# Kernel tuning notes

Measured on AMD Instinct MI355X. Metric: run time of the kernel, lower is better.

The kernel has to match this reference:

```python
import jax, jax.numpy as jnp
import numpy as np

B, IN, H1, H2, OUT, P = 8192, 1024, 2048, 2048, 1024, 8


def setup_inputs() -> dict:
    key = jax.random.key(0)
    ks = jax.random.split(key, 12)
    s = 0.02
    return {
        "x": jax.random.normal(ks[0], (B, IN), dtype=jnp.float32),
        # layer 1: P expert linears (stacked) + selector
        "W1": jax.random.normal(ks[1], (P, IN, H1), dtype=jnp.float32) * s,
        "b1": jax.random.normal(ks[2], (P, H1), dtype=jnp.float32) * s,
        "S1": jax.random.normal(ks[3], (IN, P), dtype=jnp.float32) * s,
        "sb1": jax.random.normal(ks[4], (P,), dtype=jnp.float32) * s,
        # layer 2
        "W2": jax.random.normal(ks[5], (P, H1, H2), dtype=jnp.float32) * s,
        "b2": jax.random.normal(ks[6], (P, H2), dtype=jnp.float32) * s,
        "S2": jax.random.normal(ks[7], (H1, P), dtype=jnp.float32) * s,
        "sb2": jax.random.normal(ks[8], (P,), dtype=jnp.float32) * s,
        # classifier
        "Wc": jax.random.normal(ks[9], (H2, OUT), dtype=jnp.float32) * s,
        "bc": jax.random.normal(ks[10], (OUT,), dtype=jnp.float32) * s,
    }


def _drn_layer(x, W, b, S, sb):
    # selector + softmax routing probs: [B, P]
    probs = jax.nn.softmax(x @ S + sb, axis=-1)
    # all-expert dense outputs: [B, P, O]
    outs = jnp.einsum('bi,pio->bpo', x, W) + b[None, :, :]
    # soft-weighted combine over experts
    return jnp.einsum('bpo,bp->bo', outs, probs)


def reference(x, W1, b1, S1, sb1, W2, b2, S2, sb2, Wc, bc):
    h = jax.nn.relu(_drn_layer(x, W1, b1, S1, sb1))
    h = jax.nn.relu(_drn_layer(h, W2, b2, S2, sb2))
    return h @ Wc + bc
```

## Files before the change

kernel.cpp:

```cpp
#include <hip/hip_runtime.h>
#include <hip/hip_bf16.h>

#define B_SZ   8192
#define IN_SZ  1024
#define H1_SZ  2048
#define H2_SZ  2048
#define OUT_SZ 1024
#define NP     8

typedef __bf16 bf16x8 __attribute__((ext_vector_type(8)));
typedef float  f32x4  __attribute__((ext_vector_type(4)));

__device__ __forceinline__ void async_ld16(const void* g, void* l) {
    __builtin_amdgcn_global_load_lds(
        (const __attribute__((address_space(1))) unsigned int*)g,
        (__attribute__((address_space(3))) unsigned int*)l,
        16, 0, 0);
}

__global__ void cast_bf16_k(const float* __restrict__ in, __hip_bfloat16* __restrict__ out) {
    size_t i = ((size_t)blockIdx.x * 256 + threadIdx.x) * 8;
    float4 f0 = *(const float4*)(in + i);
    float4 f1 = *(const float4*)(in + i + 4);
    __hip_bfloat16 t[8] = {
        __float2bfloat16(f0.x), __float2bfloat16(f0.y),
        __float2bfloat16(f0.z), __float2bfloat16(f0.w),
        __float2bfloat16(f1.x), __float2bfloat16(f1.y),
        __float2bfloat16(f1.z), __float2bfloat16(f1.w)};
    uint4 u4;
    __builtin_memcpy(&u4, t, 16);
    *(uint4*)(out + i) = u4;
}

__global__ void transpose_cast_k(const float* __restrict__ in, __hip_bfloat16* __restrict__ out,
                                 int K, int N) {
    __shared__ float tile[32][33];
    int n0 = blockIdx.x * 32, k0 = blockIdx.y * 32;
    int tx = threadIdx.x, ty = threadIdx.y;
#pragma unroll
    for (int j = 0; j < 4; ++j)
        tile[ty + j * 8][tx] = in[(size_t)(k0 + ty + j * 8) * N + (n0 + tx)];
    __syncthreads();
    const int kk = (tx & 15) * 2;
#pragma unroll
    for (int j = 0; j < 2; ++j) {
        int nn = ty + j * 8 + (tx >> 4) * 16;
        __hip_bfloat16 t2[2] = {__float2bfloat16(tile[kk][nn]),
                                __float2bfloat16(tile[kk + 1][nn])};
        unsigned int u;
        __builtin_memcpy(&u, t2, 4);
        *(unsigned int*)(out + (size_t)(n0 + nn) * K + (k0 + kk)) = u;
    }
}

template <typename T>
__global__ void selector_k(const T* __restrict__ in, const float* __restrict__ S,
                           const float* __restrict__ sb, float* __restrict__ probs,
                           float* __restrict__ ratT, int K) {
    int row  = blockIdx.x * blockDim.y + threadIdx.y;
    int lane = threadIdx.x;
    float acc[NP];
#pragma unroll
    for (int p = 0; p < NP; ++p) acc[p] = 0.f;
    const T* xr = in + (size_t)row * K;
    for (int k = lane; k < K; k += 64) {
        float xv;
        if constexpr (sizeof(T) == 2) xv = __bfloat162float(xr[k]);
        else                          xv = (float)xr[k];
        const float* sr = S + (size_t)k * NP;
#pragma unroll
        for (int p = 0; p < NP; ++p) acc[p] += xv * sr[p];
    }
#pragma unroll
    for (int p = 0; p < NP; ++p)
#pragma unroll
        for (int off = 32; off > 0; off >>= 1)
            acc[p] += __shfl_down(acc[p], off, 64);
    if (lane == 0) {
        float v[NP], m = -1e30f;
#pragma unroll
        for (int p = 0; p < NP; ++p) { v[p] = acc[p] + sb[p]; m = fmaxf(m, v[p]); }
        float s = 0.f;
#pragma unroll
        for (int p = 0; p < NP; ++p) { v[p] = expf(v[p] - m); s += v[p]; }
        float inv = 1.f / s;
#pragma unroll
        for (int p = 0; p < NP; ++p) probs[(size_t)row * NP + p] = v[p] * inv;
#pragma unroll
        for (int p = 0; p < NP - 1; ++p) ratT[(size_t)p * B_SZ + row] = v[p] / v[p + 1];
        ratT[(size_t)(NP - 1) * B_SZ + row] = v[NP - 1] * inv;
    }
}

template <int TPS>
__global__ __launch_bounds__(512, 2)
void drn_gemm8_k(const __hip_bfloat16* __restrict__ A, const __hip_bfloat16* __restrict__ Wt,
                 int N, int K, int Kin, const float* __restrict__ ratT,
                 const float* __restrict__ probs, const float* __restrict__ bexp,
                 __hip_bfloat16* __restrict__ C) {
    __shared__ alignas(16) char smem[131072];

    const int tid  = threadIdx.x;
    const int wid  = tid >> 6, lane = tid & 63;
    const int quad = lane >> 4, l16 = lane & 15;
    const int wr = wid >> 2, wc = wid & 3;

    const int g   = blockIdx.x;
    const int cpx = gridDim.x >> 3;
    const int wg  = (g & 7) * cpx + (g >> 3);
    const int nbn = N >> 8;
    const int mb  = wg / nbn, nb = wg % nbn;
    const int m0  = mb * 256, n0 = nb * 256;

    const int arow = tid >> 3;
    const int gsw  = ((tid & 7) ^ (arow & 7)) << 3;
    const __hip_bfloat16* Ag = A  + (size_t)(m0 + arow) * Kin + gsw;
    const __hip_bfloat16* Bg = Wt + (size_t)(n0 + arow) * K + gsw;
    const size_t r64a = (size_t)64 * Kin;
    const size_t r64b = (size_t)64 * K;
    char* aDst = smem + wid * 1024;
    char* bDst = smem + 65536 + wid * 1024;

#define STG_A(dbuf, ksrc, h) do {                                              \
    const __hip_bfloat16* s_ = Ag + (((ksrc) & (TPS - 1)) * 64) + (size_t)(2*(h)) * r64a; \
    char* d_ = aDst + (dbuf) * 32768 + (h) * 16384;                            \
    async_ld16(s_,        d_);                                                 \
    async_ld16(s_ + r64a, d_ + 8192); } while (0)
#define STG_B(dbuf, ksrc, h) do {                                              \
    const __hip_bfloat16* s_ = Bg + ((size_t)(ksrc) * 64) + (size_t)(2*(h)) * r64b; \
    char* d_ = bDst + (dbuf) * 32768 + (h) * 16384;                            \
    async_ld16(s_,        d_);                                                 \
    async_ld16(s_ + r64b, d_ + 8192); } while (0)

    const int csw  = (quad ^ (l16 & 7)) << 4;
    const int aoff = (wr * 128 + l16) * 128 + csw;
    const int boff = 65536 + (wc * 64 + l16) * 128 + csw;

#define LDA(dst, dbuf, m, k) dst = *(const bf16x8*)(smem + (dbuf) * 32768 + ((aoff ^ ((k) << 6)) + (m) * 2048))
#define LDB(dst, dbuf, n, k) dst = *(const bf16x8*)(smem + (dbuf) * 32768 + ((boff ^ ((k) << 6)) + (n) * 2048))

#define LD_A2(dbuf, mq)                               \
    LDA(af[0][0], dbuf, 2*(mq),     0); LDA(af[0][1], dbuf, 2*(mq),     1); \
    LDA(af[1][0], dbuf, 2*(mq) + 1, 0); LDA(af[1][1], dbuf, 2*(mq) + 1, 1)
#define LD_B8(dbuf)                                   \
    LDB(bfr[0][0], dbuf, 0, 0); LDB(bfr[0][1], dbuf, 0, 1); \
    LDB(bfr[1][0], dbuf, 1, 0); LDB(bfr[1][1], dbuf, 1, 1); \
    LDB(bfr[2][0], dbuf, 2, 0); LDB(bfr[2][1], dbuf, 2, 1); \
    LDB(bfr[3][0], dbuf, 3, 0); LDB(bfr[3][1], dbuf, 3, 1)

#define PH_SYNC()                                          \
    __builtin_amdgcn_s_barrier();                          \
    asm volatile("s_waitcnt lgkmcnt(0)" ::: "memory");     \
    __builtin_amdgcn_sched_barrier(0)

#define PH_MFMA(q) do {                                    \
    __builtin_amdgcn_s_setprio(1);                         \
    _Pragma("unroll")                                      \
    for (int ml = 0; ml < 2; ++ml)                         \
      _Pragma("unroll")                                    \
      for (int n_ = 0; n_ < 4; ++n_)                       \
        _Pragma("unroll")                                  \
        for (int k_ = 0; k_ < 2; ++k_)                     \
          acc[2*(q)+ml][n_] = __builtin_amdgcn_mfma_f32_16x16x32_bf16( \
              af[ml][k_], bfr[n_][k_], acc[2*(q)+ml][n_], 0, 0, 0);    \
    __builtin_amdgcn_s_setprio(0); } while (0)

#define PH_END()                                           \
    __builtin_amdgcn_s_barrier();                          \
    __builtin_amdgcn_sched_barrier(0)

#define PH_END_VM()                                        \
    asm volatile("s_waitcnt vmcnt(4)" ::: "memory");       \
    __builtin_amdgcn_s_barrier();                          \
    __builtin_amdgcn_sched_barrier(0)

    f32x4 zero = {0.f, 0.f, 0.f, 0.f};
    f32x4 acc[8][4];
#pragma unroll
    for (int m = 0; m < 8; ++m)
#pragma unroll
        for (int n = 0; n < 4; ++n) acc[m][n] = zero;

    const int NT = K >> 6;
    const int NI = NT >> 1;

    STG_A(0, 0, 0); STG_A(0, 0, 1);
    STG_B(0, 0, 0); STG_B(0, 0, 1);
    STG_B(1, 1, 0); STG_B(1, 1, 1);
    asm volatile("s_waitcnt vmcnt(4)" ::: "memory");
    __builtin_amdgcn_s_barrier();
    __builtin_amdgcn_sched_barrier(0);

    bf16x8 af[2][2], bfr[4][2];

    for (int i = 0; i < NI; ++i) {
        const int T  = 2 * i;
        const int k2 = (T + 2 < NT) ? T + 2 : NT - 1;
        const int k3 = (T + 3 < NT) ? T + 3 : NT - 1;

        LD_B8(0); LD_A2(0, 0);
        STG_A(1, T + 1, 0);
        PH_SYNC(); PH_MFMA(0); PH_END();

        LD_A2(0, 1);
        STG_A(1, T + 1, 1);
        PH_SYNC(); PH_MFMA(1); PH_END();

        LD_A2(0, 2);
        STG_B(0, k2, 0);
        PH_SYNC(); PH_MFMA(2); PH_END();

        LD_A2(0, 3);
        STG_B(0, k2, 1);
        PH_SYNC(); PH_MFMA(3); PH_END_VM();

        LD_B8(1); LD_A2(1, 0);
        STG_A(0, k2, 0);
        PH_SYNC(); PH_MFMA(0); PH_END();

        LD_A2(1, 1);
        STG_A(0, k2, 1);
        PH_SYNC(); PH_MFMA(1); PH_END();

        LD_A2(1, 2);
        STG_B(1, k3, 0);
        PH_SYNC(); PH_MFMA(2); PH_END();

        LD_A2(1, 3);
        STG_B(1, k3, 1);
        PH_SYNC(); PH_MFMA(3); PH_END_VM();

        if (((i + 1) & (TPS / 2 - 1)) == 0) {
            const int p = (i + 1) / (TPS / 2) - 1;
            const float* rp = ratT + (size_t)p * B_SZ + (m0 + wr * 128 + quad * 4);
            f32x4 rr[8];
#pragma unroll
            for (int m = 0; m < 8; ++m) rr[m] = *(const f32x4*)(rp + m * 16);
#pragma unroll
            for (int m = 0; m < 8; ++m)
#pragma unroll
                for (int n = 0; n < 4; ++n)
                    acc[m][n] *= rr[m];
        }
    }

    asm volatile("s_waitcnt vmcnt(0)" ::: "memory");

    const int colb = n0 + wc * 64 + l16;
    float bx[4][NP];
#pragma unroll
    for (int n = 0; n < 4; ++n)
#pragma unroll
        for (int p = 0; p < NP; ++p)
            bx[n][p] = bexp[(size_t)p * N + colb + n * 16];
#pragma unroll
    for (int m = 0; m < 8; ++m) {
#pragma unroll
        for (int r = 0; r < 4; ++r) {
            const int row = m0 + wr * 128 + m * 16 + quad * 4 + r;
            const float* pr = probs + (size_t)row * NP;
            f32x4 p0 = *(const f32x4*)pr;
            f32x4 p1 = *(const f32x4*)(pr + 4);
            float pv[NP] = {p0[0], p0[1], p0[2], p0[3], p1[0], p1[1], p1[2], p1[3]};
#pragma unroll
            for (int n = 0; n < 4; ++n) {
                float bsum = 0.f;
#pragma unroll
                for (int p = 0; p < NP; ++p) bsum += pv[p] * bx[n][p];
                float v = fmaxf(acc[m][n][r] + bsum, 0.f);
                C[(size_t)row * N + colb + n * 16] = __float2bfloat16(v);
            }
        }
    }
#undef STG_A
#undef STG_B
#undef LDA
#undef LDB
#undef LD_A2
#undef LD_B8
#undef PH_SYNC
#undef PH_MFMA
#undef PH_END
#undef PH_END_VM
}

__global__ __launch_bounds__(256)
void gemm_bt_k(const __hip_bfloat16* __restrict__ A, const __hip_bfloat16* __restrict__ Bt,
               int M, int N, int K, const float* __restrict__ bias, float* __restrict__ C) {
    __shared__ alignas(16) __hip_bfloat16 As[2 * 128 * 32];
    __shared__ alignas(16) __hip_bfloat16 Bs[2 * 128 * 32];
    const int tid  = threadIdx.x;
    const int wid  = tid >> 6, lane = tid & 63;
    const int quad = lane >> 4, l16 = lane & 15;
    const int waveM = (wid >> 1) << 6, waveN = (wid & 1) << 6;
    const int m0 = blockIdx.x * 128, n0 = blockIdx.y * 128;

    f32x4 zero = {0.f, 0.f, 0.f, 0.f};
    f32x4 acc[4][4];
#pragma unroll
    for (int a = 0; a < 4; ++a)
#pragma unroll
        for (int b = 0; b < 4; ++b) acc[a][b] = zero;

    const int srow = tid >> 2;
    const int skc  = (((tid & 3) ^ (srow & 3) ^ ((srow >> 2) & 3)) << 3);
    const __hip_bfloat16* Ag = A  + (size_t)(m0 + srow) * K + skc;
    const __hip_bfloat16* Bg = Bt + (size_t)(n0 + srow) * K + skc;
    const size_t rowStep = (size_t)64 * K;
    __hip_bfloat16* AsB = As + wid * 512;
    __hip_bfloat16* BsB = Bs + wid * 512;
    const int csel = (quad ^ (l16 & 3) ^ ((l16 >> 2) & 3)) << 3;

    async_ld16(Ag,           AsB);
    async_ld16(Ag + rowStep, AsB + 2048);
    async_ld16(Bg,           BsB);
    async_ld16(Bg + rowStep, BsB + 2048);

    for (int kt = 0; kt < K; kt += 32) {
        const int cur = (kt >> 5) & 1;
        __syncthreads();
        if (kt + 32 < K) {
            const int nb = (1 - cur) * 4096;
            async_ld16(Ag + kt + 32,           AsB + nb);
            async_ld16(Ag + kt + 32 + rowStep, AsB + nb + 2048);
            async_ld16(Bg + kt + 32,           BsB + nb);
            async_ld16(Bg + kt + 32 + rowStep, BsB + nb + 2048);
        }
        const __hip_bfloat16* AsC = As + cur * 4096;
        const __hip_bfloat16* BsC = Bs + cur * 4096;
        bf16x8 af[4], bfr[4];
#pragma unroll
        for (int q = 0; q < 4; ++q) {
            af[q]  = *(const bf16x8*)(AsC + (waveM + q * 16 + l16) * 32 + csel);
            bfr[q] = *(const bf16x8*)(BsC + (waveN + q * 16 + l16) * 32 + csel);
        }
#pragma unroll
        for (int tm = 0; tm < 4; ++tm)
#pragma unroll
            for (int tn = 0; tn < 4; ++tn)
                acc[tm][tn] = __builtin_amdgcn_mfma_f32_16x16x32_bf16(
                    af[tm], bfr[tn], acc[tm][tn], 0, 0, 0);
    }

    const int colb = n0 + waveN + l16;
#pragma unroll
    for (int tm = 0; tm < 4; ++tm)
#pragma unroll
        for (int r = 0; r < 4; ++r) {
            int row = m0 + waveM + tm * 16 + quad * 4 + r;
#pragma unroll
            for (int tn = 0; tn < 4; ++tn)
                C[(size_t)row * N + colb + tn * 16] =
                    acc[tm][tn][r] + bias[colb + tn * 16];
        }
}

extern "C" void kernel_launch(void* const* d_in, const int* in_sizes, int n_in,
                              void* d_out, int out_size, void* d_ws, size_t ws_size,
                              hipStream_t stream) {
    const float* x   = (const float*)d_in[0];
    const float* W1  = (const float*)d_in[1];
    const float* b1  = (const float*)d_in[2];
    const float* S1  = (const float*)d_in[3];
    const float* sb1 = (const float*)d_in[4];
    const float* W2  = (const float*)d_in[5];
    const float* b2  = (const float*)d_in[6];
    const float* S2  = (const float*)d_in[7];
    const float* sb2 = (const float*)d_in[8];
    const float* Wc  = (const float*)d_in[9];
    const float* bc  = (const float*)d_in[10];
    float* out = (float*)d_out;

    char* ws = (char*)d_ws;
    size_t off = 0;
    auto alloc = [&](size_t bytes) {
        char* p = ws + off;
        off += (bytes + 255) & ~(size_t)255;
        return p;
    };
    __hip_bfloat16* W1t = (__hip_bfloat16*)alloc((size_t)H1_SZ * (NP * IN_SZ) * 2);
    __hip_bfloat16* W2t = (__hip_bfloat16*)alloc((size_t)H2_SZ * (NP * H1_SZ) * 2);
    __hip_bfloat16* Wct = (__hip_bfloat16*)alloc((size_t)OUT_SZ * H2_SZ * 2);
    float* probs1       = (float*)alloc((size_t)B_SZ * NP * 4);
    float* probs2       = (float*)alloc((size_t)B_SZ * NP * 4);
    float* rat1         = (float*)alloc((size_t)NP * B_SZ * 4);
    float* rat2         = (float*)alloc((size_t)NP * B_SZ * 4);
    __hip_bfloat16* xbf = (__hip_bfloat16*)alloc((size_t)B_SZ * IN_SZ * 2);
    __hip_bfloat16* h1  = (__hip_bfloat16*)alloc((size_t)B_SZ * H1_SZ * 2);
    __hip_bfloat16* h2  = (__hip_bfloat16*)alloc((size_t)B_SZ * H2_SZ * 2);

    dim3 tb(32, 8);
    transpose_cast_k<<<dim3(H1_SZ / 32, (NP * IN_SZ) / 32), tb, 0, stream>>>(W1, W1t, NP * IN_SZ, H1_SZ);
    transpose_cast_k<<<dim3(H2_SZ / 32, (NP * H1_SZ) / 32), tb, 0, stream>>>(W2, W2t, NP * H1_SZ, H2_SZ);
    transpose_cast_k<<<dim3(OUT_SZ / 32, H2_SZ / 32), tb, 0, stream>>>(Wc, Wct, H2_SZ, OUT_SZ);
    cast_bf16_k<<<(B_SZ * IN_SZ) / (256 * 8), 256, 0, stream>>>(x, xbf);

    selector_k<float><<<B_SZ / 4, dim3(64, 4), 0, stream>>>(x, S1, sb1, probs1, rat1, IN_SZ);
    drn_gemm8_k<16><<<(B_SZ / 256) * (H1_SZ / 256), 512, 0, stream>>>(
        xbf, W1t, H1_SZ, NP * IN_SZ, IN_SZ, rat1, probs1, b1, h1);

    selector_k<__hip_bfloat16><<<B_SZ / 4, dim3(64, 4), 0, stream>>>(h1, S2, sb2, probs2, rat2, H1_SZ);
    drn_gemm8_k<32><<<(B_SZ / 256) * (H2_SZ / 256), 512, 0, stream>>>(
        h1, W2t, H2_SZ, NP * H1_SZ, H1_SZ, rat2, probs2, b2, h2);

    gemm_bt_k<<<dim3(B_SZ / 128, OUT_SZ / 128), 256, 0, stream>>>(
        h2, Wct, B_SZ, OUT_SZ, H2_SZ, bc, out);
}
```

Before: 1.036 ms.

## Double-buffer LDS fragment loads in DRN GEMM and merge prep kernels

Restructures the main DRN GEMM loop to ping-pong A and B register fragments, so the LDS reads for the next MFMA phase are issued before the current phase's MFMAs. It replaces the per-phase lgkmcnt(0) wait with finer-grained vmcnt waits. It also folds the three weight transpose-casts and the input cast into one prep kernel launch to cut launch overhead. In exchange the kernel uses more VGPRs for the doubled fragments, and the looser waits make the ordering of async LDS fills against reads harder to get right.

```diff
diff --git a/kernel.cpp b/kernel.cpp
--- a/kernel.cpp
+++ b/kernel.cpp
@@ -18,24 +18,11 @@
         16, 0, 0);
 }
 
-__global__ void cast_bf16_k(const float* __restrict__ in, __hip_bfloat16* __restrict__ out) {
-    size_t i = ((size_t)blockIdx.x * 256 + threadIdx.x) * 8;
-    float4 f0 = *(const float4*)(in + i);
-    float4 f1 = *(const float4*)(in + i + 4);
-    __hip_bfloat16 t[8] = {
-        __float2bfloat16(f0.x), __float2bfloat16(f0.y),
-        __float2bfloat16(f0.z), __float2bfloat16(f0.w),
-        __float2bfloat16(f1.x), __float2bfloat16(f1.y),
-        __float2bfloat16(f1.z), __float2bfloat16(f1.w)};
-    uint4 u4;
-    __builtin_memcpy(&u4, t, 16);
-    *(uint4*)(out + i) = u4;
-}
-
-__global__ void transpose_cast_k(const float* __restrict__ in, __hip_bfloat16* __restrict__ out,
-                                 int K, int N) {
-    __shared__ float tile[32][33];
-    int n0 = blockIdx.x * 32, k0 = blockIdx.y * 32;
+__device__ __forceinline__ void transpose_body(float (*tile)[33],
+                                               const float* __restrict__ in,
+                                               __hip_bfloat16* __restrict__ out,
+                                               int K, int N, int bx, int by) {
+    int n0 = bx * 32, k0 = by * 32;
     int tx = threadIdx.x, ty = threadIdx.y;
 #pragma unroll
     for (int j = 0; j < 4; ++j)
@@ -50,6 +37,46 @@
         unsigned int u;
         __builtin_memcpy(&u, t2, 4);
         *(unsigned int*)(out + (size_t)(n0 + nn) * K + (k0 + kk)) = u;
+    }
+}
+
+__global__ void prep_k(const float* __restrict__ W1, const float* __restrict__ W2,
+                       const float* __restrict__ Wc, const float* __restrict__ x,
+                       __hip_bfloat16* __restrict__ W1t, __hip_bfloat16* __restrict__ W2t,
+                       __hip_bfloat16* __restrict__ Wct, __hip_bfloat16* __restrict__ xbf) {
+    __shared__ float tile[32][33];
+    int id = blockIdx.x;
+    const int nA = (H1_SZ / 32) * ((NP * IN_SZ) / 32);
+    const int nB = (H2_SZ / 32) * ((NP * H1_SZ) / 32);
+    const int nC = (OUT_SZ / 32) * (H2_SZ / 32);
+    if (id < nA) {
+        transpose_body(tile, W1, W1t, NP * IN_SZ, H1_SZ, id % (H1_SZ / 32), id / (H1_SZ / 32));
+        return;
+    }
+    id -= nA;
+    if (id < nB) {
+        transpose_body(tile, W2, W2t, NP * H1_SZ, H2_SZ, id % (H2_SZ / 32), id / (H2_SZ / 32));
+        return;
+    }
+    id -= nB;
+    if (id < nC) {
+        transpose_body(tile, Wc, Wct, H2_SZ, OUT_SZ, id % (OUT_SZ / 32), id / (OUT_SZ / 32));
+        return;
+    }
+    id -= nC;
+    {
+        int t = threadIdx.y * 32 + threadIdx.x;
+        size_t i = ((size_t)id * 256 + t) * 8;
+        float4 f0 = *(const float4*)(x + i);
+        float4 f1 = *(const float4*)(x + i + 4);
+        __hip_bfloat16 tt[8] = {
+            __float2bfloat16(f0.x), __float2bfloat16(f0.y),
+            __float2bfloat16(f0.z), __float2bfloat16(f0.w),
+            __float2bfloat16(f1.x), __float2bfloat16(f1.y),
+            __float2bfloat16(f1.z), __float2bfloat16(f1.w)};
+        uint4 u4;
+        __builtin_memcpy(&u4, tt, 16);
+        *(uint4*)(xbf + i) = u4;
     }
 }
 
@@ -139,21 +166,20 @@
 #define LDA(dst, dbuf, m, k) dst = *(const bf16x8*)(smem + (dbuf) * 32768 + ((aoff ^ ((k) << 6)) + (m) * 2048))
 #define LDB(dst, dbuf, n, k) dst = *(const bf16x8*)(smem + (dbuf) * 32768 + ((boff ^ ((k) << 6)) + (n) * 2048))
 
-#define LD_A2(dbuf, mq)                               \
-    LDA(af[0][0], dbuf, 2*(mq),     0); LDA(af[0][1], dbuf, 2*(mq),     1); \
-    LDA(af[1][0], dbuf, 2*(mq) + 1, 0); LDA(af[1][1], dbuf, 2*(mq) + 1, 1)
-#define LD_B8(dbuf)                                   \
-    LDB(bfr[0][0], dbuf, 0, 0); LDB(bfr[0][1], dbuf, 0, 1); \
-    LDB(bfr[1][0], dbuf, 1, 0); LDB(bfr[1][1], dbuf, 1, 1); \
-    LDB(bfr[2][0], dbuf, 2, 0); LDB(bfr[2][1], dbuf, 2, 1); \
-    LDB(bfr[3][0], dbuf, 3, 0); LDB(bfr[3][1], dbuf, 3, 1)
-
-#define PH_SYNC()                                          \
+#define LD_AF(dst, dbuf, mq)                               \
+    LDA(dst[0][0], dbuf, 2*(mq),     0); LDA(dst[0][1], dbuf, 2*(mq),     1); \
+    LDA(dst[1][0], dbuf, 2*(mq) + 1, 0); LDA(dst[1][1], dbuf, 2*(mq) + 1, 1)
+#define LD_BF(dst, dbuf, kk)                               \
+    LDB(dst[0][kk], dbuf, 0, kk); LDB(dst[1][kk], dbuf, 1, kk); \
+    LDB(dst[2][kk], dbuf, 2, kk); LDB(dst[3][kk], dbuf, 3, kk)
+
+#define BAR()                                              \
     __builtin_amdgcn_s_barrier();                          \
-    asm volatile("s_waitcnt lgkmcnt(0)" ::: "memory");     \
     __builtin_amdgcn_sched_barrier(0)
 
-#define PH_MFMA(q) do {                                    \
+#define VMW(n) asm volatile("s_waitcnt vmcnt(" #n ")" ::: "memory")
+
+#define MF16(afX, bfrX, q) do {                            \
     __builtin_amdgcn_s_setprio(1);                         \
     _Pragma("unroll")                                      \
     for (int ml = 0; ml < 2; ++ml)                         \
@@ -162,17 +188,8 @@
         _Pragma("unroll")                                  \
         for (int k_ = 0; k_ < 2; ++k_)                     \
           acc[2*(q)+ml][n_] = __builtin_amdgcn_mfma_f32_16x16x32_bf16( \
-              af[ml][k_], bfr[n_][k_], acc[2*(q)+ml][n_], 0, 0, 0);    \
+              afX[ml][k_], bfrX[n_][k_], acc[2*(q)+ml][n_], 0, 0, 0);  \
     __builtin_amdgcn_s_setprio(0); } while (0)
-
-#define PH_END()                                           \
-    __builtin_amdgcn_s_barrier();                          \
-    __builtin_amdgcn_sched_barrier(0)
-
-#define PH_END_VM()                                        \
-    asm volatile("s_waitcnt vmcnt(4)" ::: "memory");       \
-    __builtin_amdgcn_s_barrier();                          \
-    __builtin_amdgcn_sched_barrier(0)
 
     f32x4 zero = {0.f, 0.f, 0.f, 0.f};
     f32x4 acc[8][4];
@@ -187,48 +204,49 @@
     STG_A(0, 0, 0); STG_A(0, 0, 1);
     STG_B(0, 0, 0); STG_B(0, 0, 1);
     STG_B(1, 1, 0); STG_B(1, 1, 1);
-    asm volatile("s_waitcnt vmcnt(4)" ::: "memory");
-    __builtin_amdgcn_s_barrier();
-    __builtin_amdgcn_sched_barrier(0);
-
-    bf16x8 af[2][2], bfr[4][2];
+    VMW(4);
+    BAR();
+    bf16x8 afA[2][2], afB[2][2], bfrA[4][2], bfrB[4][2];
+    LD_BF(bfrA, 0, 0); LD_BF(bfrA, 0, 1);
+    LD_AF(afA, 0, 0);
 
     for (int i = 0; i < NI; ++i) {
         const int T  = 2 * i;
         const int k2 = (T + 2 < NT) ? T + 2 : NT - 1;
         const int k3 = (T + 3 < NT) ? T + 3 : NT - 1;
 
-        LD_B8(0); LD_A2(0, 0);
         STG_A(1, T + 1, 0);
-        PH_SYNC(); PH_MFMA(0); PH_END();
-
-        LD_A2(0, 1);
+        LD_AF(afB, 0, 1);
+        BAR(); MF16(afA, bfrA, 0); BAR();
         STG_A(1, T + 1, 1);
-        PH_SYNC(); PH_MFMA(1); PH_END();
-
-        LD_A2(0, 2);
+        VMW(4);
+        LD_AF(afA, 0, 2);
+        BAR(); MF16(afB, bfrA, 1); BAR();
         STG_B(0, k2, 0);
-        PH_SYNC(); PH_MFMA(2); PH_END();
-
-        LD_A2(0, 3);
+        VMW(2);
+        LD_AF(afB, 0, 3);
+        LD_BF(bfrB, 1, 0);
+        BAR(); MF16(afA, bfrA, 2); BAR();
         STG_B(0, k2, 1);
-        PH_SYNC(); PH_MFMA(3); PH_END_VM();
-
-        LD_B8(1); LD_A2(1, 0);
+        LD_AF(afA, 1, 0);
+        LD_BF(bfrB, 1, 1);
+        BAR(); MF16(afB, bfrA, 3); BAR();
         STG_A(0, k2, 0);
-        PH_SYNC(); PH_MFMA(0); PH_END();
-
-        LD_A2(1, 1);
+        LD_AF(afB, 1, 1);
+        BAR(); MF16(afA, bfrB, 0); BAR();
         STG_A(0, k2, 1);
-        PH_SYNC(); PH_MFMA(1); PH_END();
-
-        LD_A2(1, 2);
+        VMW(4);
+        LD_AF(afA, 1, 2);
+        BAR(); MF16(afB, bfrB, 1); BAR();
         STG_B(1, k3, 0);
-        PH_SYNC(); PH_MFMA(2); PH_END();
-
-        LD_A2(1, 3);
+        VMW(2);
+        LD_AF(afB, 1, 3);
+        LD_BF(bfrA, 0, 0);
+        BAR(); MF16(afA, bfrB, 2); BAR();
         STG_B(1, k3, 1);
-        PH_SYNC(); PH_MFMA(3); PH_END_VM();
+        LD_AF(afA, 0, 0);
+        LD_BF(bfrA, 0, 1);
+        BAR(); MF16(afB, bfrB, 3); BAR();
 
         if (((i + 1) & (TPS / 2 - 1)) == 0) {
             const int p = (i + 1) / (TPS / 2) - 1;
@@ -276,12 +294,11 @@
 #undef STG_B
 #undef LDA
 #undef LDB
-#undef LD_A2
-#undef LD_B8
-#undef PH_SYNC
-#undef PH_MFMA
-#undef PH_END
-#undef PH_END_VM
+#undef LD_AF
+#undef LD_BF
+#undef BAR
+#undef VMW
+#undef MF16
 }
 
 __global__ __launch_bounds__(256)
@@ -389,11 +406,11 @@
     __hip_bfloat16* h1  = (__hip_bfloat16*)alloc((size_t)B_SZ * H1_SZ * 2);
     __hip_bfloat16* h2  = (__hip_bfloat16*)alloc((size_t)B_SZ * H2_SZ * 2);
 
-    dim3 tb(32, 8);
-    transpose_cast_k<<<dim3(H1_SZ / 32, (NP * IN_SZ) / 32), tb, 0, stream>>>(W1, W1t, NP * IN_SZ, H1_SZ);
-    transpose_cast_k<<<dim3(H2_SZ / 32, (NP * H1_SZ) / 32), tb, 0, stream>>>(W2, W2t, NP * H1_SZ, H2_SZ);
-    transpose_cast_k<<<dim3(OUT_SZ / 32, H2_SZ / 32), tb, 0, stream>>>(Wc, Wct, H2_SZ, OUT_SZ);
-    cast_bf16_k<<<(B_SZ * IN_SZ) / (256 * 8), 256, 0, stream>>>(x, xbf);
+    const int nPrep = (H1_SZ / 32) * ((NP * IN_SZ) / 32)
+                    + (H2_SZ / 32) * ((NP * H1_SZ) / 32)
+                    + (OUT_SZ / 32) * (H2_SZ / 32)
+                    + (B_SZ * IN_SZ) / (256 * 8);
+    prep_k<<<nPrep, dim3(32, 8), 0, stream>>>(W1, W2, Wc, x, W1t, W2t, Wct, xbf);
 
     selector_k<float><<<B_SZ / 4, dim3(64, 4), 0, stream>>>(x, S1, sb1, probs1, rat1, IN_SZ);
     drn_gemm8_k<16><<<(B_SZ / 256) * (H1_SZ / 256), 512, 0, stream>>>(
```

New measurement: 990.8 us. -4.4%, faster.
